# Performance work log

Hardware: AMD Instinct MI355X
Metric: run time of the kernel (lower is better)

## Reference

```python
import jax, jax.numpy as jnp
import numpy as np

NUM_HEADS = 16
HEAD_DIM = 64
MAX_POS = 2048


def setup_inputs() -> dict:
    key = jax.random.key(0)
    k1, k2, k3 = jax.random.split(key, 3)
    B, S, H = 2, 2048, 1024
    hidden_states = jax.random.normal(k1, (B, S, H), dtype=jnp.float32)
    attention_mask = jnp.zeros((B, 1, 1, S), dtype=jnp.float32)
    qkv_w = jax.random.normal(k2, (H, 3 * H), dtype=jnp.float32) * 0.02
    qkv_b = jnp.zeros((3 * H,), dtype=jnp.float32)
    dist_emb = jax.random.normal(k3, (2 * MAX_POS - 1, HEAD_DIM), dtype=jnp.float32) * 0.02
    return {
        "hidden_states": hidden_states,
        "attention_mask": attention_mask,
        "qkv_w": qkv_w,
        "qkv_b": qkv_b,
        "dist_emb": dist_emb,
    }


def reference(hidden_states, attention_mask, qkv_w, qkv_b, dist_emb):
    B, S, H = hidden_states.shape
    nh, hd = NUM_HEADS, HEAD_DIM
    inv_scale = 1.0 / np.sqrt(hd).astype(np.float32)

    fused = hidden_states @ qkv_w + qkv_b
    fused = fused.reshape(B, S, 3, nh, hd).transpose(2, 0, 3, 1, 4)
    q, k, v = fused[0], fused[1], fused[2]

    # Scaled QK^T scores: [B,nh,S,S]
    scores = jnp.einsum("bhqd,bhkd->bhqk", q, k) * inv_scale

    # relative_key_query positional bias
    pos = jnp.arange(S)
    distance = pos[:, None] - pos[None, :] + (MAX_POS - 1)  # [S,S] in [0, 2*MAX_POS-2]
    pos_emb = dist_emb[distance]  # [S,S,hd]
    scores = scores \
        + jnp.einsum("bhld,lrd->bhlr", q, pos_emb) \
        + jnp.einsum("bhrd,lrd->bhlr", k, pos_emb)

    # float32 softmax with additive mask (dropout prob = 0 -> identity)
    probs = jax.nn.softmax(scores.astype(jnp.float32) + attention_mask, axis=-1)
    probs = probs.astype(scores.dtype)

    # Attention-weighted values -> [B,S,H]
    ctx = jnp.einsum("bhqk,bhkd->bhqd", probs, v)
    ctx = ctx.transpose(0, 2, 1, 3).reshape(B, S, nh * hd)
    return ctx, probs
```

## Files before the change

### kernel.cpp

```cpp
#include <hip/hip_runtime.h>
#include <hip/hip_bf16.h>
#include <cstdint>

typedef __bf16 bf16;
typedef __attribute__((ext_vector_type(8))) __bf16 bf16x8;
typedef __attribute__((ext_vector_type(4))) float f32x4;
typedef __attribute__((ext_vector_type(4))) int i32x4;

static __device__ __forceinline__ f32x4 mfma16x16x32(bf16x8 a, bf16x8 b, f32x4 c) {
    return __builtin_amdgcn_mfma_f32_16x16x32_bf16(a, b, c, 0, 0, 0);
}

__global__ __launch_bounds__(256) void cvt_e_kernel(const float* __restrict__ de,
                                                    bf16* __restrict__ e) {
    int i = blockIdx.x * 256 + threadIdx.x;
    float v = (i < 4095 * 64) ? de[i] : 0.0f;
    e[i] = (bf16)v;
}

__global__ __launch_bounds__(256, 2) void qkv_gemm_kernel(
        const float* __restrict__ X, const float* __restrict__ W,
        const float* __restrict__ bias,
        bf16* __restrict__ qws, bf16* __restrict__ kws, bf16* __restrict__ vws) {
    __shared__ bf16 As[128][72];
    __shared__ bf16 Bt[128][72];
    __shared__ float BiasS[128];
    const int t = threadIdx.x;
    const int wave = t >> 6, lane = t & 63;
    const int q4 = lane >> 4, l16 = lane & 15;
    const int n0 = blockIdx.x * 128, m0 = blockIdx.y * 128;
    const int wi = wave >> 1, wj = wave & 1;

    if (t < 32) {
        f32x4 bv = *(const f32x4*)&bias[n0 + 4 * t];
        BiasS[4*t+0] = bv.x; BiasS[4*t+1] = bv.y;
        BiasS[4*t+2] = bv.z; BiasS[4*t+3] = bv.w;
    }

    f32x4 acc[4][4];
    #pragma unroll
    for (int a = 0; a < 4; ++a)
        #pragma unroll
        for (int b = 0; b < 4; ++b)
            acc[a][b] = (f32x4){0.f, 0.f, 0.f, 0.f};

    for (int kb = 0; kb < 16; ++kb) {
        const int k0 = kb * 64;
        __syncthreads();
        {
            const int r = t >> 1, ko = (t & 1) * 32;
            const float* src = &X[(size_t)(m0 + r) * 1024 + k0 + ko];
            #pragma unroll
            for (int i = 0; i < 4; ++i) {
                f32x4 v0 = *(const f32x4*)(src + 8 * i);
                f32x4 v1 = *(const f32x4*)(src + 8 * i + 4);
                bf16x8 h;
                h[0]=(bf16)v0.x; h[1]=(bf16)v0.y; h[2]=(bf16)v0.z; h[3]=(bf16)v0.w;
                h[4]=(bf16)v1.x; h[5]=(bf16)v1.y; h[6]=(bf16)v1.z; h[7]=(bf16)v1.w;
                *(bf16x8*)&As[r][ko + 8 * i] = h;
            }
        }
        {
            const int kr = t >> 2, nc = (t & 3) * 32;
            const float* src = &W[(size_t)(k0 + kr) * 3072 + n0 + nc];
            #pragma unroll
            for (int i = 0; i < 32; ++i) Bt[nc + i][kr] = (bf16)src[i];
        }
        __syncthreads();
        #pragma unroll
        for (int ks = 0; ks < 64; ks += 32) {
            bf16x8 af[4], bfr[4];
            #pragma unroll
            for (int ti = 0; ti < 4; ++ti)
                af[ti] = *(const bf16x8*)&As[wi * 64 + ti * 16 + l16][ks + q4 * 8];
            #pragma unroll
            for (int tj = 0; tj < 4; ++tj)
                bfr[tj] = *(const bf16x8*)&Bt[wj * 64 + tj * 16 + l16][ks + q4 * 8];
            #pragma unroll
            for (int ti = 0; ti < 4; ++ti)
                #pragma unroll
                for (int tj = 0; tj < 4; ++tj)
                    acc[ti][tj] = mfma16x16x32(af[ti], bfr[tj], acc[ti][tj]);
        }
    }
    #pragma unroll
    for (int ti = 0; ti < 4; ++ti) {
        #pragma unroll
        for (int tj = 0; tj < 4; ++tj) {
            const int coll = wj * 64 + tj * 16 + l16;
            const int col = n0 + coll;
            const int which = col >> 10;
            const int hh = (col >> 6) & 15;
            const int dd = col & 63;
            bf16* dst = (which == 0) ? qws : (which == 1) ? kws : vws;
            #pragma unroll
            for (int r = 0; r < 4; ++r) {
                const int row = m0 + wi * 64 + ti * 16 + q4 * 4 + r;
                const int bb = row >> 11, ss = row & 2047;
                float v = acc[ti][tj][r] + BiasS[coll];
                dst[((size_t)((bb * 16 + hh) * 2048 + ss) << 6) + dd] = (bf16)v;
            }
        }
    }
}

__global__ __launch_bounds__(256, 2) void scores_kernel(
        const bf16* __restrict__ qws, const bf16* __restrict__ kws,
        const bf16* __restrict__ ews, const float* __restrict__ mask,
        float* __restrict__ sc) {
    __shared__ bf16 Qs[64][72];
    __shared__ bf16 Ks[64][72];
    __shared__ bf16 Es[128][72];
    __shared__ bf16 QDs[64][68];
    __shared__ bf16 KDs[64][68];
    __shared__ float MskS[64];
    const int t = threadIdx.x;
    const int wave = t >> 6, lane = t & 63;
    const int q4 = lane >> 4, l16 = lane & 15;
    const int bh = blockIdx.x >> 5;
    const int l0 = (blockIdx.x & 31) << 6;
    const int bb = bh >> 4;
    const bf16* qb = qws + (size_t)bh * 2048 * 64;
    const bf16* kb = kws + (size_t)bh * 2048 * 64;
    float* scb = sc + ((size_t)bh * 2048 + l0) * 2048;

    {
        const int r = t >> 2, c = (t & 3) * 16;
        *(i32x4*)&Qs[r][c]     = *(const i32x4*)&qb[(size_t)(l0 + r) * 64 + c];
        *(i32x4*)&Qs[r][c + 8] = *(const i32x4*)&qb[(size_t)(l0 + r) * 64 + c + 8];
    }

    for (int r0 = 0; r0 < 2048; r0 += 64) {
        const int pB = l0 - r0 + 2047;
        __syncthreads();
        {
            const int r = t >> 2, c = (t & 3) * 16;
            *(i32x4*)&Ks[r][c]     = *(const i32x4*)&kb[(size_t)(r0 + r) * 64 + c];
            *(i32x4*)&Ks[r][c + 8] = *(const i32x4*)&kb[(size_t)(r0 + r) * 64 + c + 8];
        }
        {
            const int j = t >> 1, c = (t & 1) * 32;
            const bf16* src = &ews[(size_t)(pB - 63 + j) * 64 + c];
            #pragma unroll
            for (int i = 0; i < 4; ++i)
                *(i32x4*)&Es[j][c + 8 * i] = *(const i32x4*)(src + 8 * i);
        }
        if (t < 16) {
            f32x4 mv = *(const f32x4*)&mask[bb * 2048 + r0 + 4 * t];
            MskS[4*t+0]=mv.x; MskS[4*t+1]=mv.y; MskS[4*t+2]=mv.z; MskS[4*t+3]=mv.w;
        }
        __syncthreads();

        f32x4 sS[4], qd[5], kd[5];
        #pragma unroll
        for (int i = 0; i < 4; ++i) sS[i] = (f32x4){0.f,0.f,0.f,0.f};
        #pragma unroll
        for (int i = 0; i < 5; ++i) { qd[i] = (f32x4){0.f,0.f,0.f,0.f};
                                      kd[i] = (f32x4){0.f,0.f,0.f,0.f}; }
        #pragma unroll
        for (int ks = 0; ks < 64; ks += 32) {
            const bf16x8 aq = *(const bf16x8*)&Qs[wave * 16 + l16][ks + q4 * 8];
            const bf16x8 ak = *(const bf16x8*)&Ks[wave * 16 + l16][ks + q4 * 8];
            #pragma unroll
            for (int vt = 0; vt < 4; ++vt) {
                bf16x8 bk = *(const bf16x8*)&Ks[vt * 16 + l16][ks + q4 * 8];
                sS[vt] = mfma16x16x32(aq, bk, sS[vt]);
            }
            #pragma unroll
            for (int i = 0; i < 5; ++i) {
                bf16x8 be = *(const bf16x8*)&Es[(wave + i) * 16 + l16][ks + q4 * 8];
                qd[i] = mfma16x16x32(aq, be, qd[i]);
            }
            #pragma unroll
            for (int i = 0; i < 5; ++i) {
                bf16x8 be = *(const bf16x8*)&Es[(3 - wave + i) * 16 + l16][ks + q4 * 8];
                kd[i] = mfma16x16x32(ak, be, kd[i]);
            }
        }
        #pragma unroll
        for (int i = 0; i < 5; ++i) {
            #pragma unroll
            for (int r = 0; r < 4; ++r) {
                const int u  = wave * 16 + q4 * 4 + r;
                const int tq = i * 16 + l16 - (q4 * 4 + r);
                if (tq >= 0 && tq < 64) QDs[u][tq] = (bf16)qd[i][r];
                const int tk = i * 16 + l16 + (q4 * 4 + r) - 15;
                if (tk >= 0 && tk < 64) KDs[u][tk] = (bf16)kd[i][r];
            }
        }
        __syncthreads();
        #pragma unroll
        for (int vt = 0; vt < 4; ++vt) {
            #pragma unroll
            for (int r = 0; r < 4; ++r) {
                const int u = wave * 16 + q4 * 4 + r;
                const int v = vt * 16 + l16;
                float s = sS[vt][r] * 0.125f
                        + (float)QDs[u][63 - v] + (float)KDs[v][u] + MskS[v];
                scb[(size_t)u * 2048 + r0 + v] = s;
            }
        }
    }
}

__global__ __launch_bounds__(256, 2) void rowstat_kernel(
        const float* __restrict__ sc, float* __restrict__ mrow,
        float* __restrict__ lrow) {
    const int wave = threadIdx.x >> 6, lane = threadIdx.x & 63;
    const size_t row = (size_t)blockIdx.x * 4 + wave;
    const float* p = sc + row * 2048;
    f32x4 v[8];
    #pragma unroll
    for (int i = 0; i < 8; ++i) v[i] = *(const f32x4*)&p[lane * 4 + i * 256];
    float m = -3.0e38f;
    #pragma unroll
    for (int i = 0; i < 8; ++i)
        m = fmaxf(m, fmaxf(fmaxf(v[i].x, v[i].y), fmaxf(v[i].z, v[i].w)));
    #pragma unroll
    for (int d = 1; d < 64; d <<= 1) m = fmaxf(m, __shfl_xor(m, d, 64));
    float s = 0.f;
    #pragma unroll
    for (int i = 0; i < 8; ++i)
        s += __expf(v[i].x - m) + __expf(v[i].y - m)
           + __expf(v[i].z - m) + __expf(v[i].w - m);
    #pragma unroll
    for (int d = 1; d < 64; d <<= 1) s += __shfl_xor(s, d, 64);
    if (lane == 0) { mrow[row] = m; lrow[row] = s; }
}

__global__ __launch_bounds__(256, 2) void probs_pv_kernel(
        float* __restrict__ sc, const bf16* __restrict__ vws,
        const float* __restrict__ mrow, const float* __restrict__ lrow,
        float* __restrict__ out) {
    __shared__ bf16 Ps[64][72];
    __shared__ bf16 Vt[64][72];
    __shared__ float Ml[64];
    __shared__ float Rl[64];
    const int t = threadIdx.x;
    const int wave = t >> 6, lane = t & 63;
    const int q4 = lane >> 4, l16 = lane & 15;
    const int bh = blockIdx.x >> 5;
    const int l0 = (blockIdx.x & 31) << 6;
    const int bb = bh >> 4, hh = bh & 15;
    float* scb = sc + ((size_t)bh * 2048 + l0) * 2048;
    const bf16* vb = vws + (size_t)bh * 2048 * 64;
    if (t < 64) {
        Ml[t] = mrow[bh * 2048 + l0 + t];
        Rl[t] = 1.0f / lrow[bh * 2048 + l0 + t];
    }
    f32x4 acc[4];
    #pragma unroll
    for (int dt = 0; dt < 4; ++dt) acc[dt] = (f32x4){0.f,0.f,0.f,0.f};

    for (int r0 = 0; r0 < 2048; r0 += 64) {
        __syncthreads();
        {
            const int rr = t >> 2, c = (t & 3) * 16;
            float* srow = &scb[(size_t)rr * 2048 + r0 + c];
            const float mv = Ml[rr], rl = Rl[rr];
            f32x4 s0 = *(const f32x4*)(srow + 0);
            f32x4 s1 = *(const f32x4*)(srow + 4);
            f32x4 s2 = *(const f32x4*)(srow + 8);
            f32x4 s3 = *(const f32x4*)(srow + 12);
            f32x4 p0, p1, p2, p3;
            p0.x=__expf(s0.x-mv)*rl; p0.y=__expf(s0.y-mv)*rl;
            p0.z=__expf(s0.z-mv)*rl; p0.w=__expf(s0.w-mv)*rl;
            p1.x=__expf(s1.x-mv)*rl; p1.y=__expf(s1.y-mv)*rl;
            p1.z=__expf(s1.z-mv)*rl; p1.w=__expf(s1.w-mv)*rl;
            p2.x=__expf(s2.x-mv)*rl; p2.y=__expf(s2.y-mv)*rl;
            p2.z=__expf(s2.z-mv)*rl; p2.w=__expf(s2.w-mv)*rl;
            p3.x=__expf(s3.x-mv)*rl; p3.y=__expf(s3.y-mv)*rl;
            p3.z=__expf(s3.z-mv)*rl; p3.w=__expf(s3.w-mv)*rl;
            *(f32x4*)(srow + 0)  = p0;
            *(f32x4*)(srow + 4)  = p1;
            *(f32x4*)(srow + 8)  = p2;
            *(f32x4*)(srow + 12) = p3;
            bf16x8 h0, h1;
            h0[0]=(bf16)p0.x; h0[1]=(bf16)p0.y; h0[2]=(bf16)p0.z; h0[3]=(bf16)p0.w;
            h0[4]=(bf16)p1.x; h0[5]=(bf16)p1.y; h0[6]=(bf16)p1.z; h0[7]=(bf16)p1.w;
            h1[0]=(bf16)p2.x; h1[1]=(bf16)p2.y; h1[2]=(bf16)p2.z; h1[3]=(bf16)p2.w;
            h1[4]=(bf16)p3.x; h1[5]=(bf16)p3.y; h1[6]=(bf16)p3.z; h1[7]=(bf16)p3.w;
            *(bf16x8*)&Ps[rr][c]     = h0;
            *(bf16x8*)&Ps[rr][c + 8] = h1;
        }
        {
            const int vr = t >> 2, dc = (t & 3) * 16;
            bf16x8 v0 = *(const bf16x8*)&vb[(size_t)(r0 + vr) * 64 + dc];
            bf16x8 v1 = *(const bf16x8*)&vb[(size_t)(r0 + vr) * 64 + dc + 8];
            #pragma unroll
            for (int i = 0; i < 8; ++i) {
                Vt[dc + i][vr]     = v0[i];
                Vt[dc + 8 + i][vr] = v1[i];
            }
        }
        __syncthreads();
        #pragma unroll
        for (int ks = 0; ks < 64; ks += 32) {
            const bf16x8 ap = *(const bf16x8*)&Ps[wave * 16 + l16][ks + q4 * 8];
            #pragma unroll
            for (int dt = 0; dt < 4; ++dt) {
                bf16x8 bv = *(const bf16x8*)&Vt[dt * 16 + l16][ks + q4 * 8];
                acc[dt] = mfma16x16x32(ap, bv, acc[dt]);
            }
        }
    }
    #pragma unroll
    for (int dt = 0; dt < 4; ++dt) {
        #pragma unroll
        for (int r = 0; r < 4; ++r) {
            const int u = wave * 16 + q4 * 4 + r;
            const int d = dt * 16 + l16;
            out[(size_t)(bb * 2048 + l0 + u) * 1024 + hh * 64 + d] = acc[dt][r];
        }
    }
}

extern "C" void kernel_launch(void* const* d_in, const int* in_sizes, int n_in,
                              void* d_out, int out_size, void* d_ws, size_t ws_size,
                              hipStream_t stream) {
    const float* hidden = (const float*)d_in[0];
    const float* mask   = (const float*)d_in[1];
    const float* qkv_w  = (const float*)d_in[2];
    const float* qkv_b  = (const float*)d_in[3];
    const float* demb   = (const float*)d_in[4];

    float* ctx   = (float*)d_out;
    float* probs = ctx + (size_t)2 * 2048 * 1024;

    char* ws = (char*)d_ws;
    bf16*  qws  = (bf16*)(ws);
    bf16*  kws  = (bf16*)(ws + 8388608);
    bf16*  vws  = (bf16*)(ws + 16777216);
    bf16*  ews  = (bf16*)(ws + 25165824);
    float* mrow = (float*)(ws + 25690112);
    float* lrow = (float*)(ws + 25952256);

    hipLaunchKernelGGL(cvt_e_kernel, dim3(1024), dim3(256), 0, stream, demb, ews);
    hipLaunchKernelGGL(qkv_gemm_kernel, dim3(24, 32), dim3(256), 0, stream,
                       hidden, qkv_w, qkv_b, qws, kws, vws);
    hipLaunchKernelGGL(scores_kernel, dim3(1024), dim3(256), 0, stream,
                       qws, kws, ews, mask, probs);
    hipLaunchKernelGGL(rowstat_kernel, dim3(16384), dim3(256), 0, stream,
                       probs, mrow, lrow);
    hipLaunchKernelGGL(probs_pv_kernel, dim3(1024), dim3(256), 0, stream,
                       probs, vws, mrow, lrow, ctx);
}
```

Before: 1.268 ms.

## Fuse scores, row statistics and PV into one online-softmax attention kernel

Merges the scores, rowstat and probs_pv kernels into a single attention kernel. The first pass computes scores, keeps a running max and sum per row, and writes unnormalized exponentials. The second pass rescales those by a per-tile factor and multiplies by V. This removes the separate rowstat read of the whole 2048x2048 score matrix and the exp recomputation. V is now written transposed by the QKV GEMM so tiles load directly without an LDS transpose, and the K-side bias MFMA is interleaved with the Q-side one. It adds extra LDS for per-tile maxima, and the strided transposed V stores in the GEMM epilogue may be less coalesced.

```diff
diff --git a/kernel.cpp b/kernel.cpp
--- a/kernel.cpp
+++ b/kernel.cpp
@@ -92,51 +92,63 @@
             const int which = col >> 10;
             const int hh = (col >> 6) & 15;
             const int dd = col & 63;
-            bf16* dst = (which == 0) ? qws : (which == 1) ? kws : vws;
             #pragma unroll
             for (int r = 0; r < 4; ++r) {
                 const int row = m0 + wi * 64 + ti * 16 + q4 * 4 + r;
                 const int bb = row >> 11, ss = row & 2047;
                 float v = acc[ti][tj][r] + BiasS[coll];
-                dst[((size_t)((bb * 16 + hh) * 2048 + ss) << 6) + dd] = (bf16)v;
-            }
-        }
-    }
-}
-
-__global__ __launch_bounds__(256, 2) void scores_kernel(
+                if (which == 2) {
+                    vws[((size_t)((bb * 16 + hh) * 64 + dd) << 11) + ss] = (bf16)v;
+                } else {
+                    bf16* dst = which ? kws : qws;
+                    dst[((size_t)((bb * 16 + hh) * 2048 + ss) << 6) + dd] = (bf16)v;
+                }
+            }
+        }
+    }
+}
+
+__global__ __launch_bounds__(256, 2) void attn_kernel(
         const bf16* __restrict__ qws, const bf16* __restrict__ kws,
-        const bf16* __restrict__ ews, const float* __restrict__ mask,
-        float* __restrict__ sc) {
-    __shared__ bf16 Qs[64][72];
-    __shared__ bf16 Ks[64][72];
+        const bf16* __restrict__ vtws, const bf16* __restrict__ ews,
+        const float* __restrict__ mask,
+        float* __restrict__ sc, float* __restrict__ out) {
+    __shared__ bf16 QP[64][72];
+    __shared__ bf16 KV[64][72];
     __shared__ bf16 Es[128][72];
     __shared__ bf16 QDs[64][68];
     __shared__ bf16 KDs[64][68];
     __shared__ float MskS[64];
+    __shared__ float Mt[64][33];
+    __shared__ float Mrun[64];
+    __shared__ float Lrun[64];
     const int t = threadIdx.x;
     const int wave = t >> 6, lane = t & 63;
     const int q4 = lane >> 4, l16 = lane & 15;
+    const int w3 = 3 - wave;
     const int bh = blockIdx.x >> 5;
     const int l0 = (blockIdx.x & 31) << 6;
-    const int bb = bh >> 4;
+    const int bb = bh >> 4, hh = bh & 15;
     const bf16* qb = qws + (size_t)bh * 2048 * 64;
     const bf16* kb = kws + (size_t)bh * 2048 * 64;
     float* scb = sc + ((size_t)bh * 2048 + l0) * 2048;
 
+    if (t < 64) { Mrun[t] = -3.0e38f; Lrun[t] = 0.f; }
+
     {
         const int r = t >> 2, c = (t & 3) * 16;
-        *(i32x4*)&Qs[r][c]     = *(const i32x4*)&qb[(size_t)(l0 + r) * 64 + c];
-        *(i32x4*)&Qs[r][c + 8] = *(const i32x4*)&qb[(size_t)(l0 + r) * 64 + c + 8];
-    }
-
-    for (int r0 = 0; r0 < 2048; r0 += 64) {
+        *(i32x4*)&QP[r][c]     = *(const i32x4*)&qb[(size_t)(l0 + r) * 64 + c];
+        *(i32x4*)&QP[r][c + 8] = *(const i32x4*)&qb[(size_t)(l0 + r) * 64 + c + 8];
+    }
+
+    for (int it = 0; it < 32; ++it) {
+        const int r0 = it << 6;
         const int pB = l0 - r0 + 2047;
         __syncthreads();
         {
             const int r = t >> 2, c = (t & 3) * 16;
-            *(i32x4*)&Ks[r][c]     = *(const i32x4*)&kb[(size_t)(r0 + r) * 64 + c];
-            *(i32x4*)&Ks[r][c + 8] = *(const i32x4*)&kb[(size_t)(r0 + r) * 64 + c + 8];
+            *(i32x4*)&KV[r][c]     = *(const i32x4*)&kb[(size_t)(r0 + r) * 64 + c];
+            *(i32x4*)&KV[r][c + 8] = *(const i32x4*)&kb[(size_t)(r0 + r) * 64 + c + 8];
         }
         {
             const int j = t >> 1, c = (t & 1) * 32;
@@ -159,21 +171,17 @@
                                       kd[i] = (f32x4){0.f,0.f,0.f,0.f}; }
         #pragma unroll
         for (int ks = 0; ks < 64; ks += 32) {
-            const bf16x8 aq = *(const bf16x8*)&Qs[wave * 16 + l16][ks + q4 * 8];
-            const bf16x8 ak = *(const bf16x8*)&Ks[wave * 16 + l16][ks + q4 * 8];
+            const bf16x8 aq = *(const bf16x8*)&QP[wave * 16 + l16][ks + q4 * 8];
+            const bf16x8 ak = *(const bf16x8*)&KV[w3 * 16 + l16][ks + q4 * 8];
             #pragma unroll
             for (int vt = 0; vt < 4; ++vt) {
-                bf16x8 bk = *(const bf16x8*)&Ks[vt * 16 + l16][ks + q4 * 8];
+                bf16x8 bk = *(const bf16x8*)&KV[vt * 16 + l16][ks + q4 * 8];
                 sS[vt] = mfma16x16x32(aq, bk, sS[vt]);
             }
             #pragma unroll
             for (int i = 0; i < 5; ++i) {
                 bf16x8 be = *(const bf16x8*)&Es[(wave + i) * 16 + l16][ks + q4 * 8];
                 qd[i] = mfma16x16x32(aq, be, qd[i]);
-            }
-            #pragma unroll
-            for (int i = 0; i < 5; ++i) {
-                bf16x8 be = *(const bf16x8*)&Es[(3 - wave + i) * 16 + l16][ks + q4 * 8];
                 kd[i] = mfma16x16x32(ak, be, kd[i]);
             }
         }
@@ -181,96 +189,82 @@
         for (int i = 0; i < 5; ++i) {
             #pragma unroll
             for (int r = 0; r < 4; ++r) {
-                const int u  = wave * 16 + q4 * 4 + r;
+                const int uq = wave * 16 + q4 * 4 + r;
                 const int tq = i * 16 + l16 - (q4 * 4 + r);
-                if (tq >= 0 && tq < 64) QDs[u][tq] = (bf16)qd[i][r];
+                if (tq >= 0 && tq < 64) QDs[uq][tq] = (bf16)qd[i][r];
+                const int uk = w3 * 16 + q4 * 4 + r;
                 const int tk = i * 16 + l16 + (q4 * 4 + r) - 15;
-                if (tk >= 0 && tk < 64) KDs[u][tk] = (bf16)kd[i][r];
-            }
-        }
-        __syncthreads();
-        #pragma unroll
-        for (int vt = 0; vt < 4; ++vt) {
+                if (tk >= 0 && tk < 64) KDs[uk][tk] = (bf16)kd[i][r];
+            }
+        }
+        __syncthreads();
+        float sv[4][4];
+        #pragma unroll
+        for (int vt = 0; vt < 4; ++vt)
             #pragma unroll
             for (int r = 0; r < 4; ++r) {
                 const int u = wave * 16 + q4 * 4 + r;
                 const int v = vt * 16 + l16;
-                float s = sS[vt][r] * 0.125f
-                        + (float)QDs[u][63 - v] + (float)KDs[v][u] + MskS[v];
-                scb[(size_t)u * 2048 + r0 + v] = s;
-            }
-        }
-    }
-}
-
-__global__ __launch_bounds__(256, 2) void rowstat_kernel(
-        const float* __restrict__ sc, float* __restrict__ mrow,
-        float* __restrict__ lrow) {
-    const int wave = threadIdx.x >> 6, lane = threadIdx.x & 63;
-    const size_t row = (size_t)blockIdx.x * 4 + wave;
-    const float* p = sc + row * 2048;
-    f32x4 v[8];
-    #pragma unroll
-    for (int i = 0; i < 8; ++i) v[i] = *(const f32x4*)&p[lane * 4 + i * 256];
-    float m = -3.0e38f;
-    #pragma unroll
-    for (int i = 0; i < 8; ++i)
-        m = fmaxf(m, fmaxf(fmaxf(v[i].x, v[i].y), fmaxf(v[i].z, v[i].w)));
-    #pragma unroll
-    for (int d = 1; d < 64; d <<= 1) m = fmaxf(m, __shfl_xor(m, d, 64));
-    float s = 0.f;
-    #pragma unroll
-    for (int i = 0; i < 8; ++i)
-        s += __expf(v[i].x - m) + __expf(v[i].y - m)
-           + __expf(v[i].z - m) + __expf(v[i].w - m);
-    #pragma unroll
-    for (int d = 1; d < 64; d <<= 1) s += __shfl_xor(s, d, 64);
-    if (lane == 0) { mrow[row] = m; lrow[row] = s; }
-}
-
-__global__ __launch_bounds__(256, 2) void probs_pv_kernel(
-        float* __restrict__ sc, const bf16* __restrict__ vws,
-        const float* __restrict__ mrow, const float* __restrict__ lrow,
-        float* __restrict__ out) {
-    __shared__ bf16 Ps[64][72];
-    __shared__ bf16 Vt[64][72];
-    __shared__ float Ml[64];
-    __shared__ float Rl[64];
-    const int t = threadIdx.x;
-    const int wave = t >> 6, lane = t & 63;
-    const int q4 = lane >> 4, l16 = lane & 15;
-    const int bh = blockIdx.x >> 5;
-    const int l0 = (blockIdx.x & 31) << 6;
-    const int bb = bh >> 4, hh = bh & 15;
-    float* scb = sc + ((size_t)bh * 2048 + l0) * 2048;
-    const bf16* vb = vws + (size_t)bh * 2048 * 64;
+                sv[vt][r] = sS[vt][r] * 0.125f
+                          + (float)QDs[u][63 - v] + (float)KDs[v][u] + MskS[v];
+            }
+        #pragma unroll
+        for (int r = 0; r < 4; ++r) {
+            const int u = wave * 16 + q4 * 4 + r;
+            float tm = fmaxf(fmaxf(sv[0][r], sv[1][r]), fmaxf(sv[2][r], sv[3][r]));
+            tm = fmaxf(tm, __shfl_xor(tm, 1, 64));
+            tm = fmaxf(tm, __shfl_xor(tm, 2, 64));
+            tm = fmaxf(tm, __shfl_xor(tm, 4, 64));
+            tm = fmaxf(tm, __shfl_xor(tm, 8, 64));
+            const float mo = Mrun[u];
+            const float mn = fmaxf(mo, tm);
+            float ts = 0.f;
+            #pragma unroll
+            for (int vt = 0; vt < 4; ++vt) {
+                const float p = __expf(sv[vt][r] - mn);
+                scb[(size_t)u * 2048 + r0 + vt * 16 + l16] = p;
+                ts += p;
+            }
+            ts += __shfl_xor(ts, 1, 64);
+            ts += __shfl_xor(ts, 2, 64);
+            ts += __shfl_xor(ts, 4, 64);
+            ts += __shfl_xor(ts, 8, 64);
+            if (l16 == 0) {
+                Lrun[u] = Lrun[u] * __expf(mo - mn) + ts;
+                Mrun[u] = mn;
+                Mt[u][it] = mn;
+            }
+        }
+    }
+
+    __syncthreads();
     if (t < 64) {
-        Ml[t] = mrow[bh * 2048 + l0 + t];
-        Rl[t] = 1.0f / lrow[bh * 2048 + l0 + t];
-    }
+        const float mf = Mrun[t];
+        const float rl = 1.0f / Lrun[t];
+        #pragma unroll
+        for (int it = 0; it < 32; ++it)
+            Mt[t][it] = __expf(Mt[t][it] - mf) * rl;
+    }
+
     f32x4 acc[4];
     #pragma unroll
     for (int dt = 0; dt < 4; ++dt) acc[dt] = (f32x4){0.f,0.f,0.f,0.f};
 
-    for (int r0 = 0; r0 < 2048; r0 += 64) {
+    for (int it = 0; it < 32; ++it) {
+        const int r0 = it << 6;
         __syncthreads();
         {
             const int rr = t >> 2, c = (t & 3) * 16;
+            const float s = Mt[rr][it];
             float* srow = &scb[(size_t)rr * 2048 + r0 + c];
-            const float mv = Ml[rr], rl = Rl[rr];
-            f32x4 s0 = *(const f32x4*)(srow + 0);
-            f32x4 s1 = *(const f32x4*)(srow + 4);
-            f32x4 s2 = *(const f32x4*)(srow + 8);
-            f32x4 s3 = *(const f32x4*)(srow + 12);
-            f32x4 p0, p1, p2, p3;
-            p0.x=__expf(s0.x-mv)*rl; p0.y=__expf(s0.y-mv)*rl;
-            p0.z=__expf(s0.z-mv)*rl; p0.w=__expf(s0.w-mv)*rl;
-            p1.x=__expf(s1.x-mv)*rl; p1.y=__expf(s1.y-mv)*rl;
-            p1.z=__expf(s1.z-mv)*rl; p1.w=__expf(s1.w-mv)*rl;
-            p2.x=__expf(s2.x-mv)*rl; p2.y=__expf(s2.y-mv)*rl;
-            p2.z=__expf(s2.z-mv)*rl; p2.w=__expf(s2.w-mv)*rl;
-            p3.x=__expf(s3.x-mv)*rl; p3.y=__expf(s3.y-mv)*rl;
-            p3.z=__expf(s3.z-mv)*rl; p3.w=__expf(s3.w-mv)*rl;
+            f32x4 p0 = *(const f32x4*)(srow + 0);
+            f32x4 p1 = *(const f32x4*)(srow + 4);
+            f32x4 p2 = *(const f32x4*)(srow + 8);
+            f32x4 p3 = *(const f32x4*)(srow + 12);
+            p0.x*=s; p0.y*=s; p0.z*=s; p0.w*=s;
+            p1.x*=s; p1.y*=s; p1.z*=s; p1.w*=s;
+            p2.x*=s; p2.y*=s; p2.z*=s; p2.w*=s;
+            p3.x*=s; p3.y*=s; p3.z*=s; p3.w*=s;
             *(f32x4*)(srow + 0)  = p0;
             *(f32x4*)(srow + 4)  = p1;
             *(f32x4*)(srow + 8)  = p2;
@@ -280,26 +274,22 @@
             h0[4]=(bf16)p1.x; h0[5]=(bf16)p1.y; h0[6]=(bf16)p1.z; h0[7]=(bf16)p1.w;
             h1[0]=(bf16)p2.x; h1[1]=(bf16)p2.y; h1[2]=(bf16)p2.z; h1[3]=(bf16)p2.w;
             h1[4]=(bf16)p3.x; h1[5]=(bf16)p3.y; h1[6]=(bf16)p3.z; h1[7]=(bf16)p3.w;
-            *(bf16x8*)&Ps[rr][c]     = h0;
-            *(bf16x8*)&Ps[rr][c + 8] = h1;
-        }
-        {
-            const int vr = t >> 2, dc = (t & 3) * 16;
-            bf16x8 v0 = *(const bf16x8*)&vb[(size_t)(r0 + vr) * 64 + dc];
-            bf16x8 v1 = *(const bf16x8*)&vb[(size_t)(r0 + vr) * 64 + dc + 8];
-            #pragma unroll
-            for (int i = 0; i < 8; ++i) {
-                Vt[dc + i][vr]     = v0[i];
-                Vt[dc + 8 + i][vr] = v1[i];
-            }
+            *(bf16x8*)&QP[rr][c]     = h0;
+            *(bf16x8*)&QP[rr][c + 8] = h1;
+        }
+        {
+            const int dr = t >> 2, c = (t & 3) * 16;
+            const bf16* src = &vtws[(((size_t)bh * 64 + dr) << 11) + r0 + c];
+            *(i32x4*)&KV[dr][c]     = *(const i32x4*)(src);
+            *(i32x4*)&KV[dr][c + 8] = *(const i32x4*)(src + 8);
         }
         __syncthreads();
         #pragma unroll
         for (int ks = 0; ks < 64; ks += 32) {
-            const bf16x8 ap = *(const bf16x8*)&Ps[wave * 16 + l16][ks + q4 * 8];
+            const bf16x8 ap = *(const bf16x8*)&QP[wave * 16 + l16][ks + q4 * 8];
             #pragma unroll
             for (int dt = 0; dt < 4; ++dt) {
-                bf16x8 bv = *(const bf16x8*)&Vt[dt * 16 + l16][ks + q4 * 8];
+                bf16x8 bv = *(const bf16x8*)&KV[dt * 16 + l16][ks + q4 * 8];
                 acc[dt] = mfma16x16x32(ap, bv, acc[dt]);
             }
         }
@@ -330,18 +320,12 @@
     char* ws = (char*)d_ws;
     bf16*  qws  = (bf16*)(ws);
     bf16*  kws  = (bf16*)(ws + 8388608);
-    bf16*  vws  = (bf16*)(ws + 16777216);
+    bf16*  vtws = (bf16*)(ws + 16777216);
     bf16*  ews  = (bf16*)(ws + 25165824);
-    float* mrow = (float*)(ws + 25690112);
-    float* lrow = (float*)(ws + 25952256);
 
     hipLaunchKernelGGL(cvt_e_kernel, dim3(1024), dim3(256), 0, stream, demb, ews);
     hipLaunchKernelGGL(qkv_gemm_kernel, dim3(24, 32), dim3(256), 0, stream,
-                       hidden, qkv_w, qkv_b, qws, kws, vws);
-    hipLaunchKernelGGL(scores_kernel, dim3(1024), dim3(256), 0, stream,
-                       qws, kws, ews, mask, probs);
-    hipLaunchKernelGGL(rowstat_kernel, dim3(16384), dim3(256), 0, stream,
-                       probs, mrow, lrow);
-    hipLaunchKernelGGL(probs_pv_kernel, dim3(1024), dim3(256), 0, stream,
-                       probs, vws, mrow, lrow, ctx);
-}
+                       hidden, qkv_w, qkv_b, qws, kws, vtws);
+    hipLaunchKernelGGL(attn_kernel, dim3(1024), dim3(256), 0, stream,
+                       qws, kws, vtws, ews, mask, probs, ctx);
+}
```

Measured after the change: 1.109 ms. 1.14x faster.
